# Optimization experiments

Measured on AMD Instinct MI355X. Metric: run time of the kernel, lower is better.

## Reference

```python
import jax, jax.numpy as jnp
import numpy as np

N = 50000
E = 800000
F_IN = 96
HID = 96
NCLS = 40


def setup_inputs() -> dict:
    key = jax.random.key(0)
    ks = jax.random.split(key, 10)
    x = jax.random.normal(ks[0], (N, F_IN), dtype=jnp.float32)
    edge_index = jax.random.randint(ks[1], (2, E), 0, N, dtype=jnp.int64)
    def lin(k, fan_in, fan_out):
        kw, kb = jax.random.split(k)
        bound = 1.0 / np.sqrt(fan_in)
        W = jax.random.uniform(kw, (fan_in, fan_out), minval=-bound, maxval=bound, dtype=jnp.float32)
        b = jax.random.uniform(kb, (fan_out,), minval=-bound, maxval=bound, dtype=jnp.float32)
        return W, b
    W1a, b1a = lin(ks[2], F_IN, HID)
    W1b, b1b = lin(ks[3], HID, HID)
    W2a, b2a = lin(ks[4], HID, HID)
    W2b, b2b = lin(ks[5], HID, NCLS)
    return {"x": x, "edge_index": edge_index,
            "W1a": W1a, "b1a": b1a, "W1b": W1b, "b1b": b1b,
            "W2a": W2a, "b2a": b2a, "W2b": W2b, "b2b": b2b}


def _gin_conv(h, src, dst, Wa, ba, Wb, bb):
    # GINConv with eps=0: nn(x + sum_{j->i} x_j); scatter-add over edges.
    agg = jax.ops.segment_sum(h[src], dst, num_segments=N)  # [N, d]
    z = h + agg
    z = jax.nn.relu(z @ Wa + ba)
    return z @ Wb + bb


def reference(x, edge_index, W1a, b1a, W1b, b1b, W2a, b2a, W2b, b2b):
    src, dst = edge_index[0], edge_index[1]
    h = _gin_conv(x, src, dst, W1a, b1a, W1b, b1b)
    h = jax.nn.relu(h)
    out = _gin_conv(h, src, dst, W2a, b2a, W2b, b2b)  # [N, num_classes]
    return out
```

## Files before the change

### kernel.cpp

```cpp
#include <hip/hip_runtime.h>
#include <hip/hip_bf16.h>

#define NODES 50000
#define EDGES 800000
#define FDIM  96
#define NCLS  40

#define NCHK 200
#define CHKE 4000
#define NB   196
#define NCELL (NB * NCHK)
#define SCAN_BLOCKS ((NCELL + 255) / 256)

#define WT_ELEMS (4 * 96 * 96)
#define WT_BLOCKS ((WT_ELEMS + 255) / 256)
#define F2B_N4 (NODES * FDIM / 4)
#define F2B_BLOCKS ((F2B_N4 + 255) / 256)

typedef __attribute__((ext_vector_type(8))) short s8v;
typedef __attribute__((ext_vector_type(4))) float f32x4;

__device__ __forceinline__ float b2f(ushort u) {
  unsigned int x = ((unsigned int)u) << 16;
  union { unsigned int i; float f; } c; c.i = x; return c.f;
}
__device__ __forceinline__ ushort f2b(float f) {
  __hip_bfloat16 b = __float2bfloat16(f);
  return *reinterpret_cast<ushort*>(&b);
}


__global__ __launch_bounds__(256) void bin_count_kernel(const int* __restrict__ dst,
                                                        int* __restrict__ cellCnt) {
  __shared__ int hist[NB];
  int t = threadIdx.x;
  for (int i = t; i < NB; i += 256) hist[i] = 0;
  __syncthreads();
  int s = blockIdx.x * CHKE;
  for (int i = t; i < CHKE; i += 256) atomicAdd(&hist[dst[s + i] >> 8], 1);
  __syncthreads();
  for (int i = t; i < NB; i += 256) cellCnt[i * NCHK + blockIdx.x] = hist[i];
}

__global__ __launch_bounds__(256) void partial_kernel(const int* __restrict__ a, int n,
                                                      int* __restrict__ partials) {
  __shared__ int sh[256];
  int t = threadIdx.x;
  int idx = blockIdx.x * 256 + t;
  int v = (idx < n) ? a[idx] : 0;
  sh[t] = v;
  __syncthreads();
#pragma unroll
  for (int d = 1; d < 256; d <<= 1) {
    int u = (t >= d) ? sh[t - d] : 0;
    __syncthreads();
    sh[t] += u;
    __syncthreads();
  }
  if (t == 255) partials[blockIdx.x] = sh[255];
}

__global__ __launch_bounds__(256) void scan_partials_kernel(const int* __restrict__ partials,
                                                            int nb, int* __restrict__ poffs) {
  __shared__ int sh[256];
  int t = threadIdx.x;
  int v = (t < nb) ? partials[t] : 0;
  sh[t] = v;
  __syncthreads();
#pragma unroll
  for (int d = 1; d < 256; d <<= 1) {
    int u = (t >= d) ? sh[t - d] : 0;
    __syncthreads();
    sh[t] += u;
    __syncthreads();
  }
  if (t < nb) poffs[t] = sh[t] - v;
}

__global__ __launch_bounds__(256) void final_scan_kernel(const int* __restrict__ a, int n,
                                                         const int* __restrict__ poffs,
                                                         int* __restrict__ out) {
  __shared__ int sh[256];
  int t = threadIdx.x;
  int idx = blockIdx.x * 256 + t;
  int v = (idx < n) ? a[idx] : 0;
  sh[t] = v;
  __syncthreads();
#pragma unroll
  for (int d = 1; d < 256; d <<= 1) {
    int u = (t >= d) ? sh[t - d] : 0;
    __syncthreads();
    sh[t] += u;
    __syncthreads();
  }
  if (idx < n) out[idx] = poffs[blockIdx.x] + sh[t] - v;
}

__global__ __launch_bounds__(256) void bin_scatter_kernel(const int* __restrict__ src,
                                                          const int* __restrict__ dst,
                                                          const int* __restrict__ cellOff,
                                                          int* __restrict__ ebuf) {
  __shared__ int cur[NB];
  int t = threadIdx.x;
  for (int i = t; i < NB; i += 256) cur[i] = cellOff[i * NCHK + blockIdx.x];
  __syncthreads();
  int s = blockIdx.x * CHKE;
  for (int i = t; i < CHKE; i += 256) {
    int d = dst[s + i];
    int pos = atomicAdd(&cur[d >> 8], 1);
    ebuf[pos] = ((d & 255) << 16) | src[s + i];
  }
}

__global__ __launch_bounds__(256) void bucket_sort_kernel(const int* __restrict__ ebuf,
                                                          const int* __restrict__ cellOff,
                                                          int* __restrict__ row_ptr,
                                                          int* __restrict__ col) {
  __shared__ int hist[256];
  __shared__ int sh[256];
  int b = blockIdx.x;
  int t = threadIdx.x;
  int s = cellOff[b * NCHK];
  int e = (b + 1 < NB) ? cellOff[(b + 1) * NCHK] : EDGES;
  hist[t] = 0;
  __syncthreads();
  for (int i = s + t; i < e; i += 256) atomicAdd(&hist[ebuf[i] >> 16], 1);
  __syncthreads();
  int v = hist[t];
  sh[t] = v;
  __syncthreads();
#pragma unroll
  for (int d = 1; d < 256; d <<= 1) {
    int u = (t >= d) ? sh[t - d] : 0;
    __syncthreads();
    sh[t] += u;
    __syncthreads();
  }
  int excl = sh[t] - v;
  int node = (b << 8) + t;
  if (node < NODES) row_ptr[node] = s + excl;
  if (node == NODES - 1) row_ptr[NODES] = EDGES;
  hist[t] = excl;
  __syncthreads();
  for (int i = s + t; i < e; i += 256) {
    int ed = ebuf[i];
    int r = atomicAdd(&hist[ed >> 16], 1);
    col[s + r] = ed & 0xFFFF;
  }
}


__global__ void prep_kernel(const float* __restrict__ W1a, const float* __restrict__ W1b,
                            const float* __restrict__ W2a, const float* __restrict__ W2b,
                            const float* __restrict__ x,
                            ushort* __restrict__ wt, ushort* __restrict__ xb) {
  if (blockIdx.x < WT_BLOCKS) {
    int id = blockIdx.x * 256 + threadIdx.x;
    if (id >= WT_ELEMS) return;
    int m = id / (96 * 96);
    int r = (id % (96 * 96)) / 96;
    int k = id % 96;
    float v = 0.0f;
    if (m == 0) v = W1a[k * 96 + r];
    else if (m == 1) v = W1b[k * 96 + r];
    else if (m == 2) v = W2a[k * 96 + r];
    else if (r < NCLS) v = W2b[k * NCLS + r];
    wt[id] = f2b(v);
  } else {
    int i = (blockIdx.x - WT_BLOCKS) * 256 + threadIdx.x;
    if (i < F2B_N4) {
      float4 v = ((const float4*)x)[i];
      ushort4 u;
      u.x = f2b(v.x); u.y = f2b(v.y); u.z = f2b(v.z); u.w = f2b(v.w);
      ((ushort4*)xb)[i] = u;
    }
  }
}


__global__ __launch_bounds__(256) void aggregate_kernel(const ushort* __restrict__ hin,
    const int* __restrict__ row_ptr, const int* __restrict__ col, ushort* __restrict__ z) {
  int gt = blockIdx.x * blockDim.x + threadIdx.x;
  int node = gt >> 6;
  if (node >= NODES) return;
  int lane = threadIdx.x & 63;
  int l = lane & 31;
  int h = lane >> 5;

  float a0 = 0.f, a1 = 0.f, a2 = 0.f;
  if (h == 0) {
    const ushort* self = hin + (size_t)node * FDIM;
    a0 = b2f(self[l]); a1 = b2f(self[l + 32]); a2 = b2f(self[l + 64]);
  }

  int e0 = row_ptr[node];
  int e1 = row_ptr[node + 1];
  int hl = (e1 - e0 + 1) >> 1;
  int e = e0 + h * hl;
  int t = h ? e1 : (e0 + hl);

  for (; e < t; e += 8) {
    const ushort* p8[8];
    float m[8];
#pragma unroll
    for (int q = 0; q < 8; ++q) {
      int idx = e + q;
      bool ok = idx < t;
      int c = col[ok ? idx : t - 1];
      p8[q] = hin + (size_t)c * FDIM;
      m[q] = ok ? 1.0f : 0.0f;
    }
    float s0 = 0.f, s1 = 0.f, s2 = 0.f;
#pragma unroll
    for (int q = 0; q < 8; ++q) {
      s0 = fmaf(m[q], b2f(p8[q][l]), s0);
      s1 = fmaf(m[q], b2f(p8[q][l + 32]), s1);
      s2 = fmaf(m[q], b2f(p8[q][l + 64]), s2);
    }
    a0 += s0; a1 += s1; a2 += s2;
  }

  a0 += __shfl_xor(a0, 32);
  a1 += __shfl_xor(a1, 32);
  a2 += __shfl_xor(a2, 32);

  if (h == 0) {
    ushort* zp = z + (size_t)node * FDIM;
    zp[l] = f2b(a0); zp[l + 32] = f2b(a1); zp[l + 64] = f2b(a2);
  }
}


template <int NOUT2, bool RELU2, bool OUT_BF16>
__global__ __launch_bounds__(256) void gin_mlp_kernel(const ushort* __restrict__ A,
    const ushort* __restrict__ wtA, const float* __restrict__ biasA,
    const ushort* __restrict__ wtB, const float* __restrict__ biasB, void* __restrict__ outv) {
  constexpr int NT2 = (NOUT2 == 96) ? 6 : 3;
  __shared__ ushort sT[64 * 128];

  int lane = threadIdx.x & 63;
  int wave = threadIdx.x >> 6;
  int wrow0 = wave * 16;
  int node0 = blockIdx.x * 64;
  int r = lane & 15;
  int kq = lane >> 4;

  int arow = node0 + wrow0 + r;
  if (arow >= NODES) arow = NODES - 1;
  const ushort* ap = A + (size_t)arow * 96 + kq * 8;
  s8v a0 = *(const s8v*)(ap);
  s8v a1 = *(const s8v*)(ap + 32);
  s8v a2 = *(const s8v*)(ap + 64);

#pragma unroll
  for (int nt = 0; nt < 6; ++nt) {
    int colg = nt * 16 + r;
    const ushort* bp = wtA + (size_t)colg * 96 + kq * 8;
    s8v b0 = *(const s8v*)(bp);
    s8v b1 = *(const s8v*)(bp + 32);
    s8v b2 = *(const s8v*)(bp + 64);
    float bv = biasA[colg];
    f32x4 acc = {bv, bv, bv, bv};
    acc = __builtin_amdgcn_mfma_f32_16x16x32_bf16(a0, b0, acc, 0, 0, 0);
    acc = __builtin_amdgcn_mfma_f32_16x16x32_bf16(a1, b1, acc, 0, 0, 0);
    acc = __builtin_amdgcn_mfma_f32_16x16x32_bf16(a2, b2, acc, 0, 0, 0);
#pragma unroll
    for (int j = 0; j < 4; ++j) {
      int trow = wrow0 + kq * 4 + j;
      float v = fmaxf(acc[j], 0.0f);
      sT[(trow * 128) + (colg ^ ((trow & 7) << 3))] = f2b(v);
    }
  }
  __syncthreads();

  int trow = wrow0 + r;
  int sbase = trow * 128;
  int swz = (trow & 7) << 3;
  s8v c0 = *(const s8v*)&sT[sbase + ((kq * 8 + 0)  ^ swz)];
  s8v c1 = *(const s8v*)&sT[sbase + ((kq * 8 + 32) ^ swz)];
  s8v c2 = *(const s8v*)&sT[sbase + ((kq * 8 + 64) ^ swz)];

#pragma unroll
  for (int nt = 0; nt < NT2; ++nt) {
    int colg = nt * 16 + r;
    const ushort* bp = wtB + (size_t)colg * 96 + kq * 8;
    s8v b0 = *(const s8v*)(bp);
    s8v b1 = *(const s8v*)(bp + 32);
    s8v b2 = *(const s8v*)(bp + 64);
    float bv = (colg < NOUT2) ? biasB[colg] : 0.0f;
    f32x4 acc = {bv, bv, bv, bv};
    acc = __builtin_amdgcn_mfma_f32_16x16x32_bf16(c0, b0, acc, 0, 0, 0);
    acc = __builtin_amdgcn_mfma_f32_16x16x32_bf16(c1, b1, acc, 0, 0, 0);
    acc = __builtin_amdgcn_mfma_f32_16x16x32_bf16(c2, b2, acc, 0, 0, 0);
#pragma unroll
    for (int j = 0; j < 4; ++j) {
      int grow = node0 + wrow0 + kq * 4 + j;
      if (grow < NODES && colg < NOUT2) {
        float v = acc[j];
        if (RELU2) v = fmaxf(v, 0.0f);
        if (OUT_BF16)
          ((ushort*)outv)[(size_t)grow * NOUT2 + colg] = f2b(v);
        else
          ((float*)outv)[(size_t)grow * NOUT2 + colg] = v;
      }
    }
  }
}


extern "C" void kernel_launch(void* const* d_in, const int* in_sizes, int n_in,
                              void* d_out, int out_size, void* d_ws, size_t ws_size,
                              hipStream_t stream) {
  const float* x    = (const float*)d_in[0];
  const int*   ei   = (const int*)d_in[1];
  const float* W1a  = (const float*)d_in[2];
  const float* b1a  = (const float*)d_in[3];
  const float* W1b  = (const float*)d_in[4];
  const float* b1b  = (const float*)d_in[5];
  const float* W2a  = (const float*)d_in[6];
  const float* b2a  = (const float*)d_in[7];
  const float* W2b  = (const float*)d_in[8];
  const float* b2b  = (const float*)d_in[9];
  float* out = (float*)d_out;

  const int* src = ei;
  const int* dst = ei + EDGES;

  char* ws = (char*)d_ws;
  size_t off = 0;
  auto alloc = [&](size_t bytes) {
    size_t p = off;
    off = (off + bytes + 255) & ~(size_t)255;
    return p;
  };
  int*  cellCnt  = (int*)(ws + alloc((size_t)NCELL * 4));
  int*  cellOff  = (int*)(ws + alloc((size_t)NCELL * 4));
  int*  partials = (int*)(ws + alloc((size_t)SCAN_BLOCKS * 4));
  int*  poffs    = (int*)(ws + alloc((size_t)SCAN_BLOCKS * 4));
  int*  row_ptr  = (int*)(ws + alloc((size_t)(NODES + 1) * 4));
  int*  ebuf     = (int*)(ws + alloc((size_t)EDGES * 4));
  int*  col      = (int*)(ws + alloc((size_t)EDGES * 4));
  ushort* wt     = (ushort*)(ws + alloc((size_t)4 * 96 * 96 * 2));
  ushort* xb     = (ushort*)(ws + alloc((size_t)NODES * FDIM * 2));
  ushort* B1     = (ushort*)(ws + alloc((size_t)NODES * FDIM * 2));
  ushort* B2     = (ushort*)(ws + alloc((size_t)NODES * FDIM * 2));

  const int AGG_GRID  = (NODES * 64 + 255) / 256;
  const int GEMM_GRID = (NODES + 63) / 64;

  bin_count_kernel<<<NCHK, 256, 0, stream>>>(dst, cellCnt);
  partial_kernel<<<SCAN_BLOCKS, 256, 0, stream>>>(cellCnt, NCELL, partials);
  scan_partials_kernel<<<1, 256, 0, stream>>>(partials, SCAN_BLOCKS, poffs);
  final_scan_kernel<<<SCAN_BLOCKS, 256, 0, stream>>>(cellCnt, NCELL, poffs, cellOff);
  bin_scatter_kernel<<<NCHK, 256, 0, stream>>>(src, dst, cellOff, ebuf);
  bucket_sort_kernel<<<NB, 256, 0, stream>>>(ebuf, cellOff, row_ptr, col);

  prep_kernel<<<WT_BLOCKS + F2B_BLOCKS, 256, 0, stream>>>(W1a, W1b, W2a, W2b, x, wt, xb);

  aggregate_kernel<<<AGG_GRID, 256, 0, stream>>>(xb, row_ptr, col, B1);
  gin_mlp_kernel<96, true, true><<<GEMM_GRID, 256, 0, stream>>>(
      B1, wt + 0 * 9216, b1a, wt + 1 * 9216, b1b, B2);

  aggregate_kernel<<<AGG_GRID, 256, 0, stream>>>(B2, row_ptr, col, B1);
  gin_mlp_kernel<40, false, false><<<GEMM_GRID, 256, 0, stream>>>(
      B1, wt + 2 * 9216, b2a, wt + 3 * 9216, b2b, out);
}
```

Before: 122.6 us.

## Fuse CSR construction into one cooperative kernel and store col as ushort

Replaces the six CSR-building launches (bin count, three-stage scan, bin scatter, bucket sort) with one cooperative kernel of 200 blocks that uses grid-wide syncs between phases. The scan is re-partitioned into 200 segments of 196 cells so each block scans one segment. Column indices are also narrowed from int to ushort, halving the index traffic in the aggregation kernels. The cost is five grid barriers and the requirement that all 200 blocks be co-resident. The 16-bit column format only holds node ids below 65536, which fits the fixed 50000 nodes.

```diff
diff --git a/kernel.cpp b/kernel.cpp
--- a/kernel.cpp
+++ b/kernel.cpp
@@ -1,5 +1,8 @@
 #include <hip/hip_runtime.h>
 #include <hip/hip_bf16.h>
+#include <hip/hip_cooperative_groups.h>
+
+namespace cg = cooperative_groups;
 
 #define NODES 50000
 #define EDGES 800000
@@ -10,7 +13,7 @@
 #define CHKE 4000
 #define NB   196
 #define NCELL (NB * NCHK)
-#define SCAN_BLOCKS ((NCELL + 255) / 256)
+#define SEG   196
 
 #define WT_ELEMS (4 * 96 * 96)
 #define WT_BLOCKS ((WT_ELEMS + 255) / 256)
@@ -30,122 +33,105 @@
 }
 
 
-__global__ __launch_bounds__(256) void bin_count_kernel(const int* __restrict__ dst,
-                                                        int* __restrict__ cellCnt) {
-  __shared__ int hist[NB];
-  int t = threadIdx.x;
-  for (int i = t; i < NB; i += 256) hist[i] = 0;
-  __syncthreads();
-  int s = blockIdx.x * CHKE;
-  for (int i = t; i < CHKE; i += 256) atomicAdd(&hist[dst[s + i] >> 8], 1);
-  __syncthreads();
-  for (int i = t; i < NB; i += 256) cellCnt[i * NCHK + blockIdx.x] = hist[i];
-}
-
-__global__ __launch_bounds__(256) void partial_kernel(const int* __restrict__ a, int n,
-                                                      int* __restrict__ partials) {
-  __shared__ int sh[256];
-  int t = threadIdx.x;
-  int idx = blockIdx.x * 256 + t;
-  int v = (idx < n) ? a[idx] : 0;
-  sh[t] = v;
-  __syncthreads();
-#pragma unroll
-  for (int d = 1; d < 256; d <<= 1) {
-    int u = (t >= d) ? sh[t - d] : 0;
-    __syncthreads();
-    sh[t] += u;
-    __syncthreads();
-  }
-  if (t == 255) partials[blockIdx.x] = sh[255];
-}
-
-__global__ __launch_bounds__(256) void scan_partials_kernel(const int* __restrict__ partials,
-                                                            int nb, int* __restrict__ poffs) {
-  __shared__ int sh[256];
-  int t = threadIdx.x;
-  int v = (t < nb) ? partials[t] : 0;
-  sh[t] = v;
-  __syncthreads();
-#pragma unroll
-  for (int d = 1; d < 256; d <<= 1) {
-    int u = (t >= d) ? sh[t - d] : 0;
-    __syncthreads();
-    sh[t] += u;
-    __syncthreads();
-  }
-  if (t < nb) poffs[t] = sh[t] - v;
-}
-
-__global__ __launch_bounds__(256) void final_scan_kernel(const int* __restrict__ a, int n,
-                                                         const int* __restrict__ poffs,
-                                                         int* __restrict__ out) {
-  __shared__ int sh[256];
-  int t = threadIdx.x;
-  int idx = blockIdx.x * 256 + t;
-  int v = (idx < n) ? a[idx] : 0;
-  sh[t] = v;
-  __syncthreads();
-#pragma unroll
-  for (int d = 1; d < 256; d <<= 1) {
-    int u = (t >= d) ? sh[t - d] : 0;
-    __syncthreads();
-    sh[t] += u;
-    __syncthreads();
-  }
-  if (idx < n) out[idx] = poffs[blockIdx.x] + sh[t] - v;
-}
-
-__global__ __launch_bounds__(256) void bin_scatter_kernel(const int* __restrict__ src,
-                                                          const int* __restrict__ dst,
-                                                          const int* __restrict__ cellOff,
-                                                          int* __restrict__ ebuf) {
-  __shared__ int cur[NB];
-  int t = threadIdx.x;
-  for (int i = t; i < NB; i += 256) cur[i] = cellOff[i * NCHK + blockIdx.x];
-  __syncthreads();
-  int s = blockIdx.x * CHKE;
-  for (int i = t; i < CHKE; i += 256) {
-    int d = dst[s + i];
-    int pos = atomicAdd(&cur[d >> 8], 1);
-    ebuf[pos] = ((d & 255) << 16) | src[s + i];
-  }
-}
-
-__global__ __launch_bounds__(256) void bucket_sort_kernel(const int* __restrict__ ebuf,
-                                                          const int* __restrict__ cellOff,
-                                                          int* __restrict__ row_ptr,
-                                                          int* __restrict__ col) {
+__global__ __launch_bounds__(256) void coop_csr_kernel(const int* __restrict__ src,
+    const int* __restrict__ dst, int* __restrict__ cellCnt, int* __restrict__ partials,
+    int* __restrict__ poffs, int* __restrict__ cellOff, int* __restrict__ ebuf,
+    int* __restrict__ row_ptr, ushort* __restrict__ col) {
+  cg::grid_group grid = cg::this_grid();
   __shared__ int hist[256];
   __shared__ int sh[256];
-  int b = blockIdx.x;
-  int t = threadIdx.x;
-  int s = cellOff[b * NCHK];
-  int e = (b + 1 < NB) ? cellOff[(b + 1) * NCHK] : EDGES;
+  int b = blockIdx.x, t = threadIdx.x;
+
   hist[t] = 0;
   __syncthreads();
-  for (int i = s + t; i < e; i += 256) atomicAdd(&hist[ebuf[i] >> 16], 1);
+  int s0 = b * CHKE;
+  for (int i = t; i < CHKE; i += 256) atomicAdd(&hist[dst[s0 + i] >> 8], 1);
   __syncthreads();
-  int v = hist[t];
-  sh[t] = v;
+  for (int i = t; i < NB; i += 256) cellCnt[i * NCHK + b] = hist[i];
+  grid.sync();
+
+  {
+    int v = (t < SEG) ? cellCnt[b * SEG + t] : 0;
+    sh[t] = v;
+    __syncthreads();
+#pragma unroll
+    for (int d = 1; d < 256; d <<= 1) {
+      int u = (t >= d) ? sh[t - d] : 0;
+      __syncthreads();
+      sh[t] += u;
+      __syncthreads();
+    }
+    if (t == 255) partials[b] = sh[255];
+  }
+  grid.sync();
+
+  if (b == 0) {
+    int v = (t < NCHK) ? partials[t] : 0;
+    sh[t] = v;
+    __syncthreads();
+#pragma unroll
+    for (int d = 1; d < 256; d <<= 1) {
+      int u = (t >= d) ? sh[t - d] : 0;
+      __syncthreads();
+      sh[t] += u;
+      __syncthreads();
+    }
+    if (t < NCHK) poffs[t] = sh[t] - v;
+  }
+  grid.sync();
+
+  {
+    int v = (t < SEG) ? cellCnt[b * SEG + t] : 0;
+    sh[t] = v;
+    __syncthreads();
+#pragma unroll
+    for (int d = 1; d < 256; d <<= 1) {
+      int u = (t >= d) ? sh[t - d] : 0;
+      __syncthreads();
+      sh[t] += u;
+      __syncthreads();
+    }
+    if (t < SEG) cellOff[b * SEG + t] = poffs[b] + sh[t] - v;
+  }
+  grid.sync();
+
+  for (int i = t; i < NB; i += 256) hist[i] = cellOff[i * NCHK + b];
   __syncthreads();
-#pragma unroll
-  for (int d = 1; d < 256; d <<= 1) {
-    int u = (t >= d) ? sh[t - d] : 0;
-    __syncthreads();
-    sh[t] += u;
-    __syncthreads();
-  }
-  int excl = sh[t] - v;
-  int node = (b << 8) + t;
-  if (node < NODES) row_ptr[node] = s + excl;
-  if (node == NODES - 1) row_ptr[NODES] = EDGES;
-  hist[t] = excl;
-  __syncthreads();
-  for (int i = s + t; i < e; i += 256) {
-    int ed = ebuf[i];
-    int r = atomicAdd(&hist[ed >> 16], 1);
-    col[s + r] = ed & 0xFFFF;
+  for (int i = t; i < CHKE; i += 256) {
+    int d = dst[s0 + i];
+    int pos = atomicAdd(&hist[d >> 8], 1);
+    ebuf[pos] = ((d & 255) << 16) | src[s0 + i];
+  }
+  grid.sync();
+
+  if (b < NB) {
+    int s = cellOff[b * NCHK];
+    int e = (b + 1 < NB) ? cellOff[(b + 1) * NCHK] : EDGES;
+    hist[t] = 0;
+    __syncthreads();
+    for (int i = s + t; i < e; i += 256) atomicAdd(&hist[ebuf[i] >> 16], 1);
+    __syncthreads();
+    int v = hist[t];
+    sh[t] = v;
+    __syncthreads();
+#pragma unroll
+    for (int d = 1; d < 256; d <<= 1) {
+      int u = (t >= d) ? sh[t - d] : 0;
+      __syncthreads();
+      sh[t] += u;
+      __syncthreads();
+    }
+    int excl = sh[t] - v;
+    int node = (b << 8) + t;
+    if (node < NODES) row_ptr[node] = s + excl;
+    if (node == NODES - 1) row_ptr[NODES] = EDGES;
+    hist[t] = excl;
+    __syncthreads();
+    for (int i = s + t; i < e; i += 256) {
+      int ed = ebuf[i];
+      int r = atomicAdd(&hist[ed >> 16], 1);
+      col[s + r] = (ushort)(ed & 0xFFFF);
+    }
   }
 }
 
@@ -179,7 +165,7 @@
 
 
 __global__ __launch_bounds__(256) void aggregate_kernel(const ushort* __restrict__ hin,
-    const int* __restrict__ row_ptr, const int* __restrict__ col, ushort* __restrict__ z) {
+    const int* __restrict__ row_ptr, const ushort* __restrict__ col, ushort* __restrict__ z) {
   int gt = blockIdx.x * blockDim.x + threadIdx.x;
   int node = gt >> 6;
   if (node >= NODES) return;
@@ -335,11 +321,11 @@
   };
   int*  cellCnt  = (int*)(ws + alloc((size_t)NCELL * 4));
   int*  cellOff  = (int*)(ws + alloc((size_t)NCELL * 4));
-  int*  partials = (int*)(ws + alloc((size_t)SCAN_BLOCKS * 4));
-  int*  poffs    = (int*)(ws + alloc((size_t)SCAN_BLOCKS * 4));
+  int*  partials = (int*)(ws + alloc((size_t)NCHK * 4));
+  int*  poffs    = (int*)(ws + alloc((size_t)NCHK * 4));
   int*  row_ptr  = (int*)(ws + alloc((size_t)(NODES + 1) * 4));
   int*  ebuf     = (int*)(ws + alloc((size_t)EDGES * 4));
-  int*  col      = (int*)(ws + alloc((size_t)EDGES * 4));
+  ushort* col    = (ushort*)(ws + alloc((size_t)EDGES * 2));
   ushort* wt     = (ushort*)(ws + alloc((size_t)4 * 96 * 96 * 2));
   ushort* xb     = (ushort*)(ws + alloc((size_t)NODES * FDIM * 2));
   ushort* B1     = (ushort*)(ws + alloc((size_t)NODES * FDIM * 2));
@@ -348,12 +334,13 @@
   const int AGG_GRID  = (NODES * 64 + 255) / 256;
   const int GEMM_GRID = (NODES + 63) / 64;
 
-  bin_count_kernel<<<NCHK, 256, 0, stream>>>(dst, cellCnt);
-  partial_kernel<<<SCAN_BLOCKS, 256, 0, stream>>>(cellCnt, NCELL, partials);
-  scan_partials_kernel<<<1, 256, 0, stream>>>(partials, SCAN_BLOCKS, poffs);
-  final_scan_kernel<<<SCAN_BLOCKS, 256, 0, stream>>>(cellCnt, NCELL, poffs, cellOff);
-  bin_scatter_kernel<<<NCHK, 256, 0, stream>>>(src, dst, cellOff, ebuf);
-  bucket_sort_kernel<<<NB, 256, 0, stream>>>(ebuf, cellOff, row_ptr, col);
+  {
+    void* args[] = {(void*)&src, (void*)&dst, (void*)&cellCnt, (void*)&partials,
+                    (void*)&poffs, (void*)&cellOff, (void*)&ebuf, (void*)&row_ptr,
+                    (void*)&col};
+    hipLaunchCooperativeKernel((const void*)coop_csr_kernel, dim3(NCHK), dim3(256),
+                               args, 0, stream);
+  }
 
   prep_kernel<<<WT_BLOCKS + F2B_BLOCKS, 256, 0, stream>>>(W1a, W1b, W2a, W2b, x, wt, xb);
 
```

Result: slower. 246.8 us (+101.3%).
